# Kernel optimization log

Hardware: AMD Instinct MI355X
Metric: run time of the kernel (lower is better)

Reference implementation:

```python
import jax, jax.numpy as jnp
import numpy as np

EPS = 1e-4          # ReEig epsilon buffer
IN_SIZE = 4096      # input SPD matrix is IN_SIZE x IN_SIZE
HID = 5             # hard-coded bottleneck in RiemSPD
OUT_SIZE = 2048     # output SPD matrix is OUT_SIZE x OUT_SIZE


def _orthogonal(key, rows, cols):
    # mimic nn.init.orthogonal_: semi-orthogonal (rows, cols) matrix
    n, m = max(rows, cols), min(rows, cols)
    a = jax.random.normal(key, (n, m), dtype=jnp.float32)
    q, _ = jnp.linalg.qr(a)
    q = q[:, :m]
    return q if rows >= cols else q.T


def bimap(x, w):
    # BiMap.forward: W^T @ X @ W
    return w.T @ (x @ w)


def rectify(x):
    # Rectify.forward: SVD, clip singular values at EPS, rebuild u diag(s) u^T
    u, s, _ = jnp.linalg.svd(x)
    s = jnp.maximum(s, EPS)
    return (u * s[None, :]) @ u.T


def setup_inputs() -> dict:
    key = jax.random.key(0)
    k1, k2, k3 = jax.random.split(key, 3)
    X = jax.random.normal(k1, (1, IN_SIZE, IN_SIZE), dtype=jnp.float32)
    W1 = _orthogonal(k2, IN_SIZE, HID)   # encoder BiMap weight (in_size, 5)
    W2 = _orthogonal(k3, HID, OUT_SIZE)  # decoder BiMap weight (5, out_size)
    return {"X": X, "W1": W1, "W2": W2}


def reference(X, W1, W2):
    x = X[0]                       # squeeze(0): (IN_SIZE, IN_SIZE)
    y = rectify(bimap(x, W1))      # encoder: (5, 5)
    z = rectify(bimap(y, W2))      # decoder: (OUT_SIZE, OUT_SIZE)
    return z
```

## Files before the change

kernel.cpp:

```cpp
#include <hip/hip_runtime.h>
#include <math.h>

static constexpr int N   = 4096;
static constexpr int H   = 5;
static constexpr int NO  = 2048;
static constexpr float FEPS = 1e-4f;
static constexpr int NJC  = 4;
static constexpr int NIG  = 256;
static constexpr int RPB  = N / NIG;
static constexpr int NBLK = NIG * NJC;
static constexpr int NCON = 256;
static constexpr int NR   = NO / NCON;

#if __has_builtin(__builtin_amdgcn_rcpf)
__device__ __forceinline__ float frcp(float x) { return __builtin_amdgcn_rcpf(x); }
#else
__device__ __forceinline__ float frcp(float x) { return 1.0f / x; }
#endif
#if __has_builtin(__builtin_amdgcn_rsqf)
__device__ __forceinline__ float frsq(float x) { return __builtin_amdgcn_rsqf(x); }
#else
__device__ __forceinline__ float frsq(float x) { return 1.0f / sqrtf(x); }
#endif

__device__ __forceinline__ float wave_reduce(float v) {
#pragma unroll
    for (int o = 32; o > 0; o >>= 1) v += __shfl_down(v, o, 64);
    return v;
}

__global__ __launch_bounds__(256) void k_xw1(const float* __restrict__ X,
                                             const float* __restrict__ W1,
                                             float* __restrict__ Mp) {
    const int b   = blockIdx.x;
    const int ig  = b >> 2;
    const int jcb = b & 3;
    const int t   = threadIdx.x;
    const int j4  = jcb * 256 + t;
    const float4* W14 = reinterpret_cast<const float4*>(W1);

    float wf[20];
    {
        const float4 f0 = W14[5 * j4 + 0];
        const float4 f1 = W14[5 * j4 + 1];
        const float4 f2 = W14[5 * j4 + 2];
        const float4 f3 = W14[5 * j4 + 3];
        const float4 f4 = W14[5 * j4 + 4];
        wf[0]=f0.x;  wf[1]=f0.y;  wf[2]=f0.z;  wf[3]=f0.w;
        wf[4]=f1.x;  wf[5]=f1.y;  wf[6]=f1.z;  wf[7]=f1.w;
        wf[8]=f2.x;  wf[9]=f2.y;  wf[10]=f2.z; wf[11]=f2.w;
        wf[12]=f3.x; wf[13]=f3.y; wf[14]=f3.z; wf[15]=f3.w;
        wf[16]=f4.x; wf[17]=f4.y; wf[18]=f4.z; wf[19]=f4.w;
    }

    float pm[H][H];
#pragma unroll
    for (int a = 0; a < H; ++a)
#pragma unroll
        for (int bb = 0; bb < H; ++bb) pm[a][bb] = 0.f;

    const int i0 = ig * RPB;
#pragma unroll 4
    for (int r = 0; r < RPB; ++r) {
        const float4 x = reinterpret_cast<const float4*>(
                             X + (size_t)(i0 + r) * N)[j4];
        float t5[H];
#pragma unroll
        for (int a = 0; a < H; ++a)
            t5[a] = x.x * wf[a]      + x.y * wf[5 + a]
                  + x.z * wf[10 + a] + x.w * wf[15 + a];
        float w1r[H];
#pragma unroll
        for (int a = 0; a < H; ++a) w1r[a] = W1[(size_t)(i0 + r) * H + a];
#pragma unroll
        for (int a = 0; a < H; ++a)
#pragma unroll
            for (int bb = 0; bb < H; ++bb) pm[a][bb] += w1r[a] * t5[bb];
    }

    __shared__ float sm[4][25];
    {
        const int lane = t & 63, wv = t >> 6;
#pragma unroll
        for (int a = 0; a < H; ++a)
#pragma unroll
            for (int bb = 0; bb < H; ++bb) {
                const float v = wave_reduce(pm[a][bb]);
                if (lane == 0) sm[wv][a * H + bb] = v;
            }
    }
    __syncthreads();
    if (t < 25)
        Mp[b * 25 + t] = sm[0][t] + sm[1][t] + sm[2][t] + sm[3][t];
}

#define JROT(p, q)                                                            \
    {                                                                         \
        const float apq = __shfl(a, (p) * 5 + (q), 64);                       \
        const float app = __shfl(a, (p) * 5 + (p), 64);                       \
        const float aqq = __shfl(a, (q) * 5 + (q), 64);                       \
        const bool  skip =                                                    \
            (apq * apq) <= (1e-26f * (app * app + aqq * aqq) + 1e-38f);       \
        const float theta = (aqq - app) * frcp(2.0f * apq);                   \
        const float tden  = fabsf(theta) + sqrtf(theta * theta + 1.0f);       \
        const float ttv   = ((theta >= 0.0f) ? 1.0f : -1.0f) * frcp(tden);    \
        float cc = frsq(ttv * ttv + 1.0f);                                    \
        float ss = ttv * cc;                                                  \
        cc = skip ? 1.0f : cc;                                                \
        ss = skip ? 0.0f : ss;                                                \
        {                                                                     \
            const int  pr   = ((r == (p)) ? (q) : ((r == (q)) ? (p) : r));    \
            const float prt = __shfl(a, pr * 5 + c, 64);                      \
            a = (r == (p)) ? (cc * a - ss * prt)                              \
                           : ((r == (q)) ? (ss * prt + cc * a) : a);          \
        }                                                                     \
        {                                                                     \
            const int  pc   = ((c == (p)) ? (q) : ((c == (q)) ? (p) : c));    \
            const float prt = __shfl(a, r * 5 + pc, 64);                      \
            a = (c == (p)) ? (cc * a - ss * prt)                              \
                           : ((c == (q)) ? (ss * prt + cc * a) : a);          \
            const float urt = __shfl(u, r * 5 + pc, 64);                      \
            u = (c == (p)) ? (cc * u - ss * urt)                              \
                           : ((c == (q)) ? (ss * urt + cc * u) : u);          \
        }                                                                     \
    }

__global__ __launch_bounds__(256) void k_out(const float* __restrict__ Mp,
                                             const float* __restrict__ W2,
                                             float* __restrict__ Z) {
    __shared__ float sred[10][26];
    __shared__ float Msum[25];
    __shared__ float ys[25];
    const int t = threadIdx.x;

    if (t < 250) {
        const int e = t % 25, g = t / 25;
        float s = 0.f;
#pragma unroll 8
        for (int p = g; p < NBLK; p += 10) s += Mp[p * 25 + e];
        sred[g][e] = s;
    }
    __syncthreads();
    if (t < 25) {
        float s = 0.f;
#pragma unroll
        for (int g = 0; g < 10; ++g) s += sred[g][t];
        Msum[t] = s;
    }
    __syncthreads();

    if (t < 64) {
        const int r = t / 5, c = t % 5;
        const float m = (t < 25) ? Msum[t] : 0.f;
        float a = 0.f;
#pragma unroll
        for (int k = 0; k < H; ++k)
            a += __shfl(m, r * 5 + k, 64) * __shfl(m, c * 5 + k, 64);
        float u = (t < 25 && r == c) ? 1.0f : 0.0f;

        for (int sweep = 0; sweep < 6; ++sweep) {
            JROT(0, 1) JROT(0, 2) JROT(0, 3) JROT(0, 4) JROT(1, 2)
            JROT(1, 3) JROT(1, 4) JROT(2, 3) JROT(2, 4) JROT(3, 4)
        }

        const float ev = fmaxf(sqrtf(fmaxf(a, 0.0f)), FEPS);
        float yv = 0.f;
#pragma unroll
        for (int k = 0; k < H; ++k) {
            const float evk = __shfl(ev, 6 * k, 64);
            const float urk = __shfl(u, r * 5 + k, 64);
            const float uck = __shfl(u, c * 5 + k, 64);
            yv += evk * urk * uck;
        }
        if (t < 25) ys[t] = yv - ((r == c) ? FEPS : 0.f);
    }
    __syncthreads();

    const int i0 = blockIdx.x * NR;
    float cmat[NR][H];
#pragma unroll
    for (int r = 0; r < NR; ++r) {
        float wcol[H];
#pragma unroll
        for (int k = 0; k < H; ++k) wcol[k] = W2[(size_t)k * NO + i0 + r];
#pragma unroll
        for (int m = 0; m < H; ++m) {
            float s = 0.f;
#pragma unroll
            for (int k = 0; k < H; ++k) s += wcol[k] * ys[k * H + m];
            cmat[r][m] = s;
        }
    }

#pragma unroll
    for (int hh = 0; hh < 2; ++hh) {
        const int jj = (hh * 256 + t) * 4;
        float4 w2j[H];
#pragma unroll
        for (int m = 0; m < H; ++m)
            w2j[m] = *reinterpret_cast<const float4*>(W2 + (size_t)m * NO + jj);
#pragma unroll
        for (int r = 0; r < NR; ++r) {
            const int i = i0 + r;
            float zx = 0.f, zy = 0.f, zz = 0.f, zw = 0.f;
#pragma unroll
            for (int m = 0; m < H; ++m) {
                const float cm = cmat[r][m];
                zx += cm * w2j[m].x;
                zy += cm * w2j[m].y;
                zz += cm * w2j[m].z;
                zw += cm * w2j[m].w;
            }
            if (i >= jj && i < jj + 4) {
                if      (i == jj + 0) zx += FEPS;
                else if (i == jj + 1) zy += FEPS;
                else if (i == jj + 2) zz += FEPS;
                else                  zw += FEPS;
            }
            *reinterpret_cast<float4*>(Z + (size_t)i * NO + jj) =
                make_float4(zx, zy, zz, zw);
        }
    }
}

extern "C" void kernel_launch(void* const* d_in, const int* in_sizes, int n_in,
                              void* d_out, int out_size, void* d_ws, size_t ws_size,
                              hipStream_t stream) {
    const float* X  = (const float*)d_in[0];
    const float* W1 = (const float*)d_in[1];
    const float* W2 = (const float*)d_in[2];
    float* out = (float*)d_out;
    float* ws  = (float*)d_ws;

    float* Mp = ws;

    hipLaunchKernelGGL(k_xw1, dim3(NBLK), dim3(256), 0, stream, X, W1, Mp);
    hipLaunchKernelGGL(k_out, dim3(NCON), dim3(256), 0, stream, Mp, W2, out);
}
```

Before: 45.60 us.

## Restructure X*W1 pass into grid-strided fully unrolled loads with more blocks

The first-stage kernel now launches 2048 blocks, each covering a grid-strided set of float4 elements, instead of 1024 blocks that each walk 16 consecutive rows. All eight X loads per thread are issued up front into registers, so more memory requests are in flight before any arithmetic starts. The aim is better latency hiding on the 64 MB streaming read of X. It raises register pressure and doubles the number of partial 5x5 results that the later reduction has to combine.

```diff
diff --git a/kernel.cpp b/kernel.cpp
--- a/kernel.cpp
+++ b/kernel.cpp
@@ -1,14 +1,13 @@
 #include <hip/hip_runtime.h>
 #include <math.h>
 
-static constexpr int N   = 4096;
-static constexpr int H   = 5;
-static constexpr int NO  = 2048;
+static constexpr int N    = 4096;
+static constexpr int H    = 5;
+static constexpr int NO   = 2048;
 static constexpr float FEPS = 1e-4f;
-static constexpr int NJC  = 4;
-static constexpr int NIG  = 256;
-static constexpr int RPB  = N / NIG;
-static constexpr int NBLK = NIG * NJC;
+static constexpr int NBLK = 2048;
+static constexpr int ITER = (N * N / 4) / (NBLK * 256);
+static constexpr int STRD = NBLK * 256;
 static constexpr int NCON = 256;
 static constexpr int NR   = NO / NCON;
 
@@ -32,20 +31,20 @@
 __global__ __launch_bounds__(256) void k_xw1(const float* __restrict__ X,
                                              const float* __restrict__ W1,
                                              float* __restrict__ Mp) {
-    const int b   = blockIdx.x;
-    const int ig  = b >> 2;
-    const int jcb = b & 3;
-    const int t   = threadIdx.x;
-    const int j4  = jcb * 256 + t;
+    const int b = blockIdx.x;
+    const int t = threadIdx.x;
+    const int rowbase = b >> 2;
+    const int j4c = ((b & 3) << 8) | t;
     const float4* W14 = reinterpret_cast<const float4*>(W1);
+    const float4* X4  = reinterpret_cast<const float4*>(X);
 
     float wf[20];
     {
-        const float4 f0 = W14[5 * j4 + 0];
-        const float4 f1 = W14[5 * j4 + 1];
-        const float4 f2 = W14[5 * j4 + 2];
-        const float4 f3 = W14[5 * j4 + 3];
-        const float4 f4 = W14[5 * j4 + 4];
+        const float4 f0 = W14[5 * j4c + 0];
+        const float4 f1 = W14[5 * j4c + 1];
+        const float4 f2 = W14[5 * j4c + 2];
+        const float4 f3 = W14[5 * j4c + 3];
+        const float4 f4 = W14[5 * j4c + 4];
         wf[0]=f0.x;  wf[1]=f0.y;  wf[2]=f0.z;  wf[3]=f0.w;
         wf[4]=f1.x;  wf[5]=f1.y;  wf[6]=f1.z;  wf[7]=f1.w;
         wf[8]=f2.x;  wf[9]=f2.y;  wf[10]=f2.z; wf[11]=f2.w;
@@ -53,17 +52,22 @@
         wf[16]=f4.x; wf[17]=f4.y; wf[18]=f4.z; wf[19]=f4.w;
     }
 
+    const size_t f0i = (size_t)b * 256 + t;
+    float4 xv[ITER];
+#pragma unroll
+    for (int k = 0; k < ITER; ++k)
+        xv[k] = X4[f0i + (size_t)k * STRD];
+
     float pm[H][H];
 #pragma unroll
     for (int a = 0; a < H; ++a)
 #pragma unroll
         for (int bb = 0; bb < H; ++bb) pm[a][bb] = 0.f;
 
-    const int i0 = ig * RPB;
-#pragma unroll 4
-    for (int r = 0; r < RPB; ++r) {
-        const float4 x = reinterpret_cast<const float4*>(
-                             X + (size_t)(i0 + r) * N)[j4];
+#pragma unroll
+    for (int k = 0; k < ITER; ++k) {
+        const int row = rowbase + k * 512;
+        const float4 x = xv[k];
         float t5[H];
 #pragma unroll
         for (int a = 0; a < H; ++a)
@@ -71,7 +75,7 @@
                   + x.z * wf[10 + a] + x.w * wf[15 + a];
         float w1r[H];
 #pragma unroll
-        for (int a = 0; a < H; ++a) w1r[a] = W1[(size_t)(i0 + r) * H + a];
+        for (int a = 0; a < H; ++a) w1r[a] = W1[(size_t)row * H + a];
 #pragma unroll
         for (int a = 0; a < H; ++a)
 #pragma unroll
```

New measurement: 52.50 us. 1.15x slower.
